# Optimization experiments

Measured on AMD Instinct MI355X. Metric: run time of the kernel, lower is better.

## Reference

```python
import jax, jax.numpy as jnp
import numpy as np

B, C1, C2, H, W = 4, 96, 96, 40, 40
DE, DI, R, N, K, E, TOPK = 192, 192, 6, 16, 4, 4, 2
EPS_BN = 1e-5
EPS_LN = 1e-5


def conv1x1(x, w):
    # x: (B,C,H,W), w: (O,C)
    return jnp.einsum('bchw,oc->bohw', x, w)


def dwconv3(x, w, b):
    # depthwise 3x3, w: (C,1,3,3)
    C = x.shape[1]
    y = jax.lax.conv_general_dilated(x, w, (1, 1), 'SAME',
                                     dimension_numbers=('NCHW', 'OIHW', 'NCHW'),
                                     feature_group_count=C)
    return y + b[None, :, None, None]


def bn_eval(x, g, b):
    # BatchNorm2d in eval mode with running_mean=0, running_var=1
    s = g / jnp.sqrt(1.0 + EPS_BN)
    return x * s[None, :, None, None] + b[None, :, None, None]


def layernorm(x, g, b):
    m = x.mean(-1, keepdims=True)
    xc = x - m
    v = (xc * xc).mean(-1, keepdims=True)
    return xc / jnp.sqrt(v + EPS_LN) * g + b


def gelu(x):
    return jax.nn.gelu(x, approximate=False)


def selective_scan(xs, dts, As, Bs, Cs):
    # xs, dts: (B,K,D,L); As: (K,D,N); Bs, Cs: (B,K,N,L)
    Bb, Kk, Dd, L = xs.shape
    Nn = As.shape[-1]
    xs_l = jnp.moveaxis(xs, -1, 0)   # (L,B,K,D)
    dts_l = jnp.moveaxis(dts, -1, 0)
    Bs_l = jnp.moveaxis(Bs, -1, 0)   # (L,B,K,N)
    Cs_l = jnp.moveaxis(Cs, -1, 0)
    h0 = jnp.zeros((Bb, Kk, Dd, Nn), xs.dtype)

    def step(h, inp):
        x_t, dt_t, B_t, C_t = inp
        dA = jnp.exp(dt_t[..., None] * As)                  # (B,K,D,N)
        h = h * dA + (dt_t * x_t)[..., None] * B_t[:, :, None, :]
        y = jnp.einsum('bkdn,bkn->bkd', h, C_t)
        return h, y

    _, ys = jax.lax.scan(step, h0, (xs_l, dts_l, Bs_l, Cs_l))
    return jnp.moveaxis(ys, 0, -1)   # (B,K,D,L)


def ss2d(x, in_proj_w, conv_w, conv_b, x_proj_w, dt_w, dt_b, A_logs, Ds,
         onorm_g, onorm_b, out_proj_w):
    # x: (B, C2, H, W)
    xz = conv1x1(x, in_proj_w)                      # (B, 2*DE, H, W)
    xx, z = jnp.split(xz, 2, axis=1)
    z1 = gelu(z)
    xx = gelu(dwconv3(xx, conv_w, conv_b))          # (B, DE, H, W)

    Bb, Dd, Hh, Ww = xx.shape
    L = Hh * Ww
    x_hw = xx.reshape(Bb, Dd, L)
    x_wh = xx.transpose(0, 1, 3, 2).reshape(Bb, Dd, L)
    xs = jnp.stack([x_hw, x_wh, x_hw[..., ::-1], x_wh[..., ::-1]], axis=1)  # (B,K,D,L)

    x_dbl = jnp.einsum('bkdl,kcd->bkcl', xs, x_proj_w)
    dts_r = x_dbl[:, :, :R]
    Bs = x_dbl[:, :, R:R + N]
    Cs = x_dbl[:, :, R + N:]
    dts = jnp.einsum('bkrl,kdr->bkdl', dts_r, dt_w)
    dts = jax.nn.softplus(dts + dt_b[None, :, :, None])
    As = -jnp.exp(A_logs.reshape(K, Dd, N))

    ys = selective_scan(xs, dts, As, Bs, Cs)
    ys = ys + Ds.reshape(K, Dd)[None, :, :, None] * xs

    # CrossMerge
    y = ys[:, 0] + ys[:, 2, :, ::-1]
    y_wh = ys[:, 1] + ys[:, 3, :, ::-1]
    y = y + y_wh.reshape(Bb, Dd, Ww, Hh).transpose(0, 1, 3, 2).reshape(Bb, Dd, L)

    y = layernorm(y.transpose(0, 2, 1), onorm_g, onorm_b)   # (B,L,D)
    y = y.reshape(Bb, Hh, Ww, Dd).transpose(0, 3, 1, 2)     # (B,D,H,W)
    y = y * z1
    return conv1x1(y, out_proj_w)


def moe(x, router_w, router_b, dw_w, dw_b, pw_w, pw_b):
    Bb = x.shape[0]
    g = x.mean(axis=(2, 3))                                 # (B,C)
    logits = g @ router_w.T + router_b
    prob = jax.nn.softmax(logits / 2.0, axis=-1)
    tp, ti = jax.lax.top_k(prob, TOPK)
    tp = tp / tp.sum(-1, keepdims=True)
    wmat = jnp.zeros((Bb, E), x.dtype).at[jnp.arange(Bb)[:, None], ti].add(tp)
    out = jnp.zeros_like(x)
    for e in range(E):
        h = gelu(dwconv3(x, dw_w[e], dw_b[e]))
        h = conv1x1(h, pw_w[e]) + pw_b[e][None, :, None, None]
        out = out + wmat[:, e][:, None, None, None] * h
    return out


def _forward(x, proj_w, bn0_g, bn0_b, ls_fc1_w, ls_fc1_b, ls_bn_g, ls_bn_b,
             ls_fc2_w, ls_fc2_b, ls_fc3_w, ls_fc3_b, n1_g, n1_b,
             in_proj_w, conv_w, conv_b, x_proj_w, dt_w, dt_b, A_logs, Ds,
             onorm_g, onorm_b, out_proj_w, n2_g, n2_b,
             router_w, router_b, moe_dw_w, moe_dw_b, moe_pw_w, moe_pw_b):
    x = jax.nn.silu(bn_eval(conv1x1(x, proj_w), bn0_g, bn0_b))
    res1 = x
    # LSBlock
    h = dwconv3(x, ls_fc1_w, ls_fc1_b)
    h = bn_eval(h, ls_bn_g, ls_bn_b)
    h = conv1x1(h, ls_fc2_w) + ls_fc2_b[None, :, None, None]
    h = gelu(h)
    h = conv1x1(h, ls_fc3_w) + ls_fc3_b[None, :, None, None]
    x1 = x + h
    x1 = ss2d(bn_eval(x1, n1_g, n1_b), in_proj_w, conv_w, conv_b, x_proj_w,
              dt_w, dt_b, A_logs, Ds, onorm_g, onorm_b, out_proj_w)
    x = res1 + x1
    x2 = moe(bn_eval(x, n2_g, n2_b), router_w, router_b,
             moe_dw_w, moe_dw_b, moe_pw_w, moe_pw_b)
    return x + x2


def setup_inputs() -> dict:
    key = jax.random.key(0)
    ks = jax.random.split(key, 16)
    rn = lambda k, shape, s: jax.random.normal(k, shape, jnp.float32) * s
    ones = lambda *s: jnp.ones(s, jnp.float32)
    zeros = lambda *s: jnp.zeros(s, jnp.float32)
    return {
        'x': jax.random.normal(ks[0], (B, C1, H, W), jnp.float32),
        'proj_w': rn(ks[1], (C2, C1), 0.1),
        'bn0_g': ones(C2), 'bn0_b': zeros(C2),
        'ls_fc1_w': rn(ks[2], (C2, 1, 3, 3), 0.2), 'ls_fc1_b': zeros(C2),
        'ls_bn_g': ones(C2), 'ls_bn_b': zeros(C2),
        'ls_fc2_w': rn(ks[3], (C2, C2), 0.1), 'ls_fc2_b': zeros(C2),
        'ls_fc3_w': rn(ks[4], (C2, C2), 0.1), 'ls_fc3_b': zeros(C2),
        'n1_g': ones(C2), 'n1_b': zeros(C2),
        'in_proj_w': rn(ks[5], (2 * DE, C2), 0.1),
        'conv_w': rn(ks[6], (DE, 1, 3, 3), 0.2), 'conv_b': zeros(DE),
        'x_proj_w': rn(ks[7], (K, R + 2 * N, DI), 0.1),
        'dt_w': rn(ks[8], (K, DI, R), 0.3),
        'dt_b': rn(ks[9], (K, DI), 0.5),
        'A_logs': rn(ks[10], (K * DI, N), 0.5),
        'Ds': ones(K * DI),
        'onorm_g': ones(DI), 'onorm_b': zeros(DI),
        'out_proj_w': rn(ks[11], (C2, DE), 0.1),
        'n2_g': ones(C2), 'n2_b': zeros(C2),
        'router_w': rn(ks[12], (E, C2), 0.1), 'router_b': zeros(E),
        'moe_dw_w': rn(ks[13], (E, C2, 1, 3, 3), 0.2), 'moe_dw_b': zeros(E, C2),
        'moe_pw_w': rn(ks[14], (E, C2, C2), 0.1), 'moe_pw_b': zeros(E, C2),
    }


def reference(x, proj_w, bn0_g, bn0_b, ls_fc1_w, ls_fc1_b, ls_bn_g, ls_bn_b,
              ls_fc2_w, ls_fc2_b, ls_fc3_w, ls_fc3_b, n1_g, n1_b,
              in_proj_w, conv_w, conv_b, x_proj_w, dt_w, dt_b, A_logs, Ds,
              onorm_g, onorm_b, out_proj_w, n2_g, n2_b,
              router_w, router_b, moe_dw_w, moe_dw_b, moe_pw_w, moe_pw_b):
    return _forward(x, proj_w, bn0_g, bn0_b, ls_fc1_w, ls_fc1_b, ls_bn_g, ls_bn_b,
                    ls_fc2_w, ls_fc2_b, ls_fc3_w, ls_fc3_b, n1_g, n1_b,
                    in_proj_w, conv_w, conv_b, x_proj_w, dt_w, dt_b, A_logs, Ds,
                    onorm_g, onorm_b, out_proj_w, n2_g, n2_b,
                    router_w, router_b, moe_dw_w, moe_dw_b, moe_pw_w, moe_pw_b)
```

## Files before the change

### kernel.cpp

```cpp
#include <hip/hip_runtime.h>
#include <hip/hip_bf16.h>
#include <math.h>

#define BB 4
#define CC 96
#define LL 1600
#define DD 192
#define KK 4
#define RR 6
#define NN 16
#define EE 4
#define NCH 40
#define CLEN 40

typedef __hip_bfloat16 bf16;

__device__ __forceinline__ float geluf(float x){ return 0.5f*x*(1.0f+erff(x*0.70710678118654752440f)); }
__device__ __forceinline__ float softplusf(float x){ return (x>20.0f)? x : __logf(1.0f+__expf(x)); }
#define BNS rsqrtf(1.0f + 1e-5f)
#define LOG2E 1.44269504088896340736f

__device__ __forceinline__ int xpos(int k, int l){
  if (k==0) return l;
  if (k==2) return LL-1-l;
  int t = (k==1)? l : (LL-1-l);
  return (t%40)*40 + t/40;
}

struct P33 { const void* p[33]; };
#define NTOT 790660
__device__ const int g_cum[34] = {
  0, 614400, 623616, 623712, 623808, 624672, 624768, 624864, 624960,
  634176, 634272, 643488, 643584, 643680, 643776, 680640, 682368, 682560,
  711744, 716352, 717120, 729408, 730176, 730368, 730560, 748992, 749088,
  749184, 749568, 749572, 753028, 753412, 790276, 790660
};

__global__ void k_convert(P33 ps, float* cv){
  bool f32 = (((const unsigned*)ps.p[21])[0] == 0x3F800000u);
  int idx = blockIdx.x*256 + threadIdx.x;
  if (idx >= NTOT) return;
  int lo=0, hi=33;
  while (lo+1<hi){ int mid=(lo+hi)>>1; if (idx >= g_cum[mid]) lo=mid; else hi=mid; }
  int local = idx - g_cum[lo];
  float v = f32 ? ((const float*)ps.p[lo])[local]
                : __bfloat162float(((const bf16*)ps.p[lo])[local]);
  cv[idx] = v;
}

__global__ void k_proj(const float* x, const float* w, const float* g, const float* b_, float* out){
  __shared__ float lx[96*64];
  int bid = blockIdx.x;
  int ot = bid%3, lt = (bid/3)%25, b = bid/75;
  int l0 = lt*64, ob = ot*32;
  const float* inb = x + b*CC*LL;
  for (int i=threadIdx.x; i<96*64; i+=256) lx[i] = inb[(i>>6)*LL + l0 + (i&63)];
  __syncthreads();
  int oq = threadIdx.x>>5, lq = threadIdx.x&31;
  float acc[4][2] = {};
  #pragma unroll 4
  for (int c=0;c<96;c++){
    float x0 = lx[c*64+lq], x1 = lx[c*64+lq+32];
    #pragma unroll
    for (int jo=0;jo<4;jo++){
      float wv = w[(ob+oq+8*jo)*CC + c];
      acc[jo][0] += wv*x0; acc[jo][1] += wv*x1;
    }
  }
  #pragma unroll
  for (int jo=0;jo<4;jo++){
    int o = ob+oq+8*jo;
    float sc = g[o]*BNS, bb = b_[o];
    #pragma unroll
    for (int jl=0;jl<2;jl++){
      float v = acc[jo][jl]*sc + bb;
      out[(b*CC+o)*LL + l0+lq+32*jl] = v/(1.0f+__expf(-v));
    }
  }
}

__global__ void k_fc_gelu(const float* in, const float* w, const float* bias, float* out){
  __shared__ float lx[96*64];
  int bid = blockIdx.x;
  int ot = bid%3, lt = (bid/3)%25, b = bid/75;
  int l0 = lt*64, ob = ot*32;
  const float* inb = in + b*CC*LL;
  for (int i=threadIdx.x; i<96*64; i+=256) lx[i] = inb[(i>>6)*LL + l0 + (i&63)];
  __syncthreads();
  int oq = threadIdx.x>>5, lq = threadIdx.x&31;
  float acc[4][2] = {};
  #pragma unroll 4
  for (int c=0;c<96;c++){
    float x0 = lx[c*64+lq], x1 = lx[c*64+lq+32];
    #pragma unroll
    for (int jo=0;jo<4;jo++){
      float wv = w[(ob+oq+8*jo)*CC + c];
      acc[jo][0] += wv*x0; acc[jo][1] += wv*x1;
    }
  }
  #pragma unroll
  for (int jo=0;jo<4;jo++){
    int o = ob+oq+8*jo;
    float bb = bias[o];
    out[(b*CC+o)*LL + l0+lq]    = geluf(acc[jo][0]+bb);
    out[(b*CC+o)*LL + l0+lq+32] = geluf(acc[jo][1]+bb);
  }
}

__global__ void k_fc_res_bn(const float* in, const float* w, const float* bias, const float* res,
                            const float* g, const float* b_, float* out){
  __shared__ float lx[96*64];
  int bid = blockIdx.x;
  int ot = bid%3, lt = (bid/3)%25, b = bid/75;
  int l0 = lt*64, ob = ot*32;
  const float* inb = in + b*CC*LL;
  for (int i=threadIdx.x; i<96*64; i+=256) lx[i] = inb[(i>>6)*LL + l0 + (i&63)];
  __syncthreads();
  int oq = threadIdx.x>>5, lq = threadIdx.x&31;
  float acc[4][2] = {};
  #pragma unroll 4
  for (int c=0;c<96;c++){
    float x0 = lx[c*64+lq], x1 = lx[c*64+lq+32];
    #pragma unroll
    for (int jo=0;jo<4;jo++){
      float wv = w[(ob+oq+8*jo)*CC + c];
      acc[jo][0] += wv*x0; acc[jo][1] += wv*x1;
    }
  }
  #pragma unroll
  for (int jo=0;jo<4;jo++){
    int o = ob+oq+8*jo;
    float bb = bias[o], sc = g[o]*BNS, b2 = b_[o];
    #pragma unroll
    for (int jl=0;jl<2;jl++){
      int pos = (b*CC+o)*LL + l0+lq+32*jl;
      float v = acc[jo][jl] + bb + res[pos];
      out[pos] = v*sc + b2;
    }
  }
}

__global__ void k_inproj(const float* in, const float* w, float* xxp, float* z1){
  __shared__ float lx[96*64];
  int bid = blockIdx.x;
  int ot = bid%12, lt = (bid/12)%25, b = bid/300;
  int l0 = lt*64, ob = ot*32;
  const float* inb = in + b*CC*LL;
  for (int i=threadIdx.x; i<96*64; i+=256) lx[i] = inb[(i>>6)*LL + l0 + (i&63)];
  __syncthreads();
  int oq = threadIdx.x>>5, lq = threadIdx.x&31;
  float acc[4][2] = {};
  #pragma unroll 4
  for (int c=0;c<96;c++){
    float x0 = lx[c*64+lq], x1 = lx[c*64+lq+32];
    #pragma unroll
    for (int jo=0;jo<4;jo++){
      float wv = w[(ob+oq+8*jo)*CC + c];
      acc[jo][0] += wv*x0; acc[jo][1] += wv*x1;
    }
  }
  if (ot < 6){
    #pragma unroll
    for (int jo=0;jo<4;jo++){
      int oc = ob+oq+8*jo;
      xxp[(b*DD+oc)*LL + l0+lq]    = acc[jo][0];
      xxp[(b*DD+oc)*LL + l0+lq+32] = acc[jo][1];
    }
  } else {
    __syncthreads();
    #pragma unroll
    for (int jo=0;jo<4;jo++){
      int oo = oq+8*jo;
      lx[lq*33 + oo]      = geluf(acc[jo][0]);
      lx[(lq+32)*33 + oo] = geluf(acc[jo][1]);
    }
    __syncthreads();
    int zb = ob - 192;
    for (int i=threadIdx.x; i<64*32; i+=256){
      int u = i>>5, oo = i&31;
      z1[(b*LL + l0+u)*DD + zb + oo] = lx[u*33 + oo];
    }
  }
}

__global__ void k_ssconv(const float* in, const float* w, const float* bias, float* out){
  int idx = blockIdx.x*256 + threadIdx.x;
  if (idx >= BB*DD*LL) return;
  int l = idx%LL, d = (idx/LL)%DD, b = idx/(LL*DD);
  int y = l/40, x0 = l%40;
  const float* ip = in + (b*DD+d)*LL;
  float acc = 0.f;
  #pragma unroll
  for (int ky=0;ky<3;ky++){
    int yy = y+ky-1; if (yy<0||yy>=40) continue;
    #pragma unroll
    for (int kx=0;kx<3;kx++){
      int xx = x0+kx-1; if (xx<0||xx>=40) continue;
      acc += w[d*9+ky*3+kx] * ip[yy*40+xx];
    }
  }
  out[idx] = geluf(acc + bias[d]);
}

__global__ void k_dwbn(const float* in, const float* w, const float* bias, const float* g, const float* b_, float* out){
  int idx = blockIdx.x*256 + threadIdx.x;
  if (idx >= BB*CC*LL) return;
  int l = idx%LL, c = (idx/LL)%CC, b = idx/(LL*CC);
  int y = l/40, x0 = l%40;
  const float* ip = in + (b*CC+c)*LL;
  float acc = 0.f;
  #pragma unroll
  for (int ky=0;ky<3;ky++){
    int yy = y+ky-1; if (yy<0||yy>=40) continue;
    #pragma unroll
    for (int kx=0;kx<3;kx++){
      int xx = x0+kx-1; if (xx<0||xx>=40) continue;
      acc += w[c*9+ky*3+kx] * ip[yy*40+xx];
    }
  }
  acc += bias[c];
  out[idx] = acc*(g[c]*BNS) + b_[c];
}

__global__ void k_xs(const float* xx, float* xs){
  __shared__ float t[32][33];
  int bid = blockIdx.x;
  int lt = bid % 50, dt = (bid/50)%6, b = bid/300;
  int l0 = lt*32, d0 = dt*32;
  int tx = threadIdx.x & 31, ty = threadIdx.x >> 5;
  #pragma unroll
  for (int j=0;j<4;j++){
    int dd = ty + 8*j;
    t[dd][tx] = xx[(b*DD + d0+dd)*LL + l0 + tx];
  }
  __syncthreads();
  #pragma unroll
  for (int j=0;j<4;j++){
    int ll = ty + 8*j;
    int l = l0 + ll;
    float v = t[tx][ll];
    int lw = (l%40)*40 + l/40;
    xs[((b*2+0)*LL + l )*DD + d0 + tx] = v;
    xs[((b*2+1)*LL + lw)*DD + d0 + tx] = v;
  }
}

__global__ void k_xw(const float* xx, float* xw1){
  __shared__ float sm[40*41];
  int bd = blockIdx.x;
  const float* ip = xx + bd*LL;
  float* op = xw1 + bd*LL;
  for (int i=threadIdx.x; i<LL; i+=256) sm[(i/40)*41 + (i%40)] = ip[i];
  __syncthreads();
  for (int i=threadIdx.x; i<LL; i+=256) op[i] = sm[(i%40)*41 + (i/40)];
}

__global__ void k_xdbl(const float* xx, const float* xw1, const float* w, float* xd){
  __shared__ float lt_[64*41];
  int bid = blockIdx.x;
  int tt = bid % 25, bk = bid / 25;
  int k = bk & 3, b = bk >> 2;
  int t0 = tt*64;
  int cg = threadIdx.x >> 6, tl = threadIdx.x & 63;
  int t = t0 + tl;
  int row = (k<2)? t : (LL-1-t);
  const float* base = ((k&1)? xw1 : xx) + b*DD*LL + row;
  const float* wp[10];
  #pragma unroll
  for (int j=0;j<10;j++){
    int c = cg + 4*j; if (c>37) c = 37;
    wp[j] = w + (k*38+c)*DD;
  }
  float acc[10] = {};
  for (int d=0; d<DD; d++){
    float xv = base[d*LL];
    #pragma unroll
    for (int j=0;j<10;j++) acc[j] += wp[j][d]*xv;
  }
  #pragma unroll
  for (int j=0;j<10;j++){
    int c = cg + 4*j;
    if (c < 38) lt_[tl*41 + c] = acc[j];
  }
  __syncthreads();
  float* ob = xd + (bk*LL + t0)*38;
  for (int i=threadIdx.x; i<64*38; i+=256) ob[i] = lt_[(i/38)*41 + (i%38)];
}

__global__ void k_scan1(const float* xs, const float* xd, const float* dtw, const float* dtb,
                        const float* Alog, float* Pb, float* Sb){
  int idx = blockIdx.x*256 + threadIdx.x;
  int lane = idx & 63;
  int d16 = lane & 15, g = lane >> 4;
  int wv_ = (idx>>6) % 12;
  int rest = (idx>>6) / 12;
  int c = rest % NCH, bk = rest / NCH;
  int d = wv_*16 + d16;
  int k = bk & 3, b = bk >> 2;
  int kd = k*DD + d;
  float w6[RR];
  #pragma unroll
  for (int r=0;r<RR;r++) w6[r] = dtw[kd*RR+r];
  float bias = dtb[kd];
  float A2[4], P[4]={1.f,1.f,1.f,1.f}, S[4]={0.f,0.f,0.f,0.f};
  #pragma unroll
  for (int n=0;n<4;n++) A2[n] = -expf(Alog[kd*NN + g*4 + n])*LOG2E;
  const float* xsb = xs + ((b*2)+(k&1))*LL*DD;
  const float* xr = xd + (bk*LL + c*CLEN)*38;
  bool rev = (k>=2);
  int t0 = c*CLEN;
  for (int j=0;j<CLEN;j++){
    int t = t0+j;
    int row = rev? (LL-1-t) : t;
    float dtr = bias;
    #pragma unroll
    for (int r=0;r<RR;r++) dtr += w6[r]*xr[r];
    float dt = softplusf(dtr);
    float xv = xsb[row*DD + d];
    float u = dt*xv;
    #pragma unroll
    for (int n=0;n<4;n++){
      float dA = exp2f(dt*A2[n]);
      P[n] *= dA;
      S[n] = S[n]*dA + u*xr[RR + g*4 + n];
    }
    xr += 38;
  }
  int off = ((bk*DD + d)*NCH + c)*NN + g*4;
  *(float4*)(Pb+off) = make_float4(P[0],P[1],P[2],P[3]);
  *(float4*)(Sb+off) = make_float4(S[0],S[1],S[2],S[3]);
}

__global__ void k_scanmid(float* Pb, const float* Sb){
  int idx = blockIdx.x*256 + threadIdx.x;
  if (idx >= BB*KK*DD*NN) return;
  int n = idx%NN, bkd = idx/NN;
  float h = 0.f;
  for (int c=0;c<NCH;c++){
    int o = (bkd*NCH + c)*NN + n;
    float p = Pb[o], s = Sb[o];
    Pb[o] = h;
    h = p*h + s;
  }
}

__global__ void k_scan2(const float* xs, const float* xd, const float* dtw, const float* dtb,
                        const float* Alog, const float* Hin, const float* Ds, float* Y){
  int idx = blockIdx.x*256 + threadIdx.x;
  int lane = idx & 63;
  int d16 = lane & 15, g = lane >> 4;
  int wv_ = (idx>>6) % 12;
  int rest = (idx>>6) / 12;
  int c = rest % NCH, bk = rest / NCH;
  int d = wv_*16 + d16;
  int k = bk & 3, b = bk >> 2;
  int kd = k*DD + d;
  float w6[RR];
  #pragma unroll
  for (int r=0;r<RR;r++) w6[r] = dtw[kd*RR+r];
  float bias = dtb[kd];
  int off = ((bk*DD + d)*NCH + c)*NN + g*4;
  float4 h4 = *(const float4*)(Hin+off);
  float h[4] = {h4.x, h4.y, h4.z, h4.w};
  float A2[4];
  #pragma unroll
  for (int n=0;n<4;n++) A2[n] = -expf(Alog[kd*NN + g*4 + n])*LOG2E;
  float Dv = Ds[kd];
  const float* xsb = xs + ((b*2)+(k&1))*LL*DD;
  const float* xr = xd + (bk*LL + c*CLEN)*38;
  float* yb = Y + b*LL*DD;
  bool rev = (k>=2);
  int t0 = c*CLEN;
  for (int j=0;j<CLEN;j++){
    int t = t0+j;
    int row = rev? (LL-1-t) : t;
    float dtr = bias;
    #pragma unroll
    for (int r=0;r<RR;r++) dtr += w6[r]*xr[r];
    float dt = softplusf(dtr);
    float xv = xsb[row*DD + d];
    float u = dt*xv;
    float y = 0.f;
    #pragma unroll
    for (int n=0;n<4;n++){
      float dA = exp2f(dt*A2[n]);
      h[n] = h[n]*dA + u*xr[RR + g*4 + n];
      y += h[n]*xr[RR + NN + g*4 + n];
    }
    y += __shfl_xor(y, 16, 64);
    y += __shfl_xor(y, 32, 64);
    if (g==0){
      int p = xpos(k, t);
      atomicAdd(&yb[p*DD + d], y + Dv*xv);
    }
    xr += 38;
  }
}

__global__ void k_ln(const float* Y, const float* og, const float* ob, const float* z1, float* yz){
  int r = blockIdx.x*4 + (threadIdx.x >> 6);
  int lane = threadIdx.x & 63;
  const float* yp = Y + r*DD;
  float v0 = yp[lane], v1 = yp[lane+64], v2 = yp[lane+128];
  float s = v0+v1+v2;
  #pragma unroll
  for (int off=32; off>0; off>>=1) s += __shfl_xor(s, off, 64);
  float m = s*(1.0f/DD);
  float t0=v0-m, t1=v1-m, t2=v2-m;
  float vv = t0*t0+t1*t1+t2*t2;
  #pragma unroll
  for (int off=32; off>0; off>>=1) vv += __shfl_xor(vv, off, 64);
  float rs = rsqrtf(vv*(1.0f/DD) + 1e-5f);
  #pragma unroll
  for (int i=0;i<3;i++){
    int d = lane + 64*i;
    float t = (i==0?t0:(i==1?t1:t2));
    yz[r*DD + d] = (t*rs*og[d] + ob[d]) * z1[r*DD + d];
  }
}

__global__ void k_outproj(const float* yz, const float* w, const float* res, const float* g, const float* b_,
                          float* x2, float* xb){
  __shared__ float lx[64*193];
  int bid = blockIdx.x;
  int ot = bid%3, lt = (bid/3)%25, b = bid/75;
  int l0 = lt*64, ob = ot*32;
  const float* src = yz + (b*LL + l0)*DD;
  for (int i=threadIdx.x; i<64*192; i+=256) lx[(i/192)*193 + (i%192)] = src[i];
  __syncthreads();
  int oq = threadIdx.x>>5, lq = threadIdx.x&31;
  float acc[4][2] = {};
  #pragma unroll 4
  for (int c=0;c<192;c++){
    float x0 = lx[lq*193 + c], x1 = lx[(lq+32)*193 + c];
    #pragma unroll
    for (int jo=0;jo<4;jo++){
      float wv = w[(ob+oq+8*jo)*DD + c];
      acc[jo][0] += wv*x0; acc[jo][1] += wv*x1;
    }
  }
  #pragma unroll
  for (int jo=0;jo<4;jo++){
    int o = ob+oq+8*jo;
    float sc = g[o]*BNS, b2 = b_[o];
    #pragma unroll
    for (int jl=0;jl<2;jl++){
      int pos = (b*CC+o)*LL + l0+lq+32*jl;
      float v = res[pos] + acc[jo][jl];
      x2[pos] = v;
      xb[pos] = v*sc + b2;
    }
  }
}

__global__ void k_gmean(const float* xb, float* gv){
  __shared__ float sm[4];
  int bc = blockIdx.x;
  int tid = threadIdx.x;
  const float* p = xb + bc*LL;
  float s = 0.f;
  for (int l=tid; l<LL; l+=256) s += p[l];
  #pragma unroll
  for (int off=32; off>0; off>>=1) s += __shfl_xor(s, off, 64);
  if ((tid&63)==0) sm[tid>>6] = s;
  __syncthreads();
  if (tid==0) gv[bc] = (sm[0]+sm[1]+sm[2]+sm[3])*(1.0f/LL);
}

__global__ void k_router(const float* gv, const float* rw, const float* rb, float* wm){
  int b = threadIdx.x;
  if (b >= BB) return;
  float lg[EE];
  for (int e=0;e<EE;e++){
    float a = rb[e];
    for (int c=0;c<CC;c++) a += gv[b*CC+c]*rw[e*CC+c];
    lg[e] = a*0.5f;
  }
  float mx = lg[0];
  for (int e=1;e<EE;e++) mx = fmaxf(mx, lg[e]);
  float p[EE], s = 0.f;
  for (int e=0;e<EE;e++){ p[e] = __expf(lg[e]-mx); s += p[e]; }
  for (int e=0;e<EE;e++) p[e] /= s;
  int i1 = 0;
  for (int e=1;e<EE;e++) if (p[e] > p[i1]) i1 = e;
  int i2 = -1;
  for (int e=0;e<EE;e++){ if (e==i1) continue; if (i2<0 || p[e]>p[i2]) i2 = e; }
  float tot = p[i1]+p[i2];
  for (int e=0;e<EE;e++) wm[b*EE+e] = 0.f;
  wm[b*EE+i1] = p[i1]/tot;
  wm[b*EE+i2] = p[i2]/tot;
}

__global__ void k_moedw(const float* xb, const float* dw, const float* db, const float* wm, float* he){
  int idx = blockIdx.x*256 + threadIdx.x;
  if (idx >= EE*BB*CC*LL) return;
  int l = idx%LL, c = (idx/LL)%CC, b = (idx/(LL*CC))%BB, e = idx/(LL*CC*BB);
  if (wm[b*EE+e] == 0.f) return;
  int y = l/40, x0 = l%40;
  const float* ip = xb + (b*CC+c)*LL;
  float acc = 0.f;
  #pragma unroll
  for (int ky=0;ky<3;ky++){
    int yy = y+ky-1; if (yy<0||yy>=40) continue;
    #pragma unroll
    for (int kx=0;kx<3;kx++){
      int xx = x0+kx-1; if (xx<0||xx>=40) continue;
      acc += dw[(e*CC+c)*9+ky*3+kx] * ip[yy*40+xx];
    }
  }
  he[((e*BB+b)*CC+c)*LL+l] = geluf(acc + db[e*CC+c]);
}

__global__ void k_final(const float* he, const float* pw, const float* pb, const float* wm,
                        const float* x2, void* out, const void* dsraw){
  __shared__ float lx[96*64];
  bool f32 = (((const unsigned*)dsraw)[0] == 0x3F800000u);
  int bid = blockIdx.x;
  int ot = bid%3, lt = (bid/3)%25, b = bid/75;
  int l0 = lt*64, ob = ot*32;
  int oq = threadIdx.x>>5, lq = threadIdx.x&31;
  float acc[4][2] = {};
  float bias[4] = {0.f,0.f,0.f,0.f};
  for (int e=0;e<EE;e++){
    float wv = wm[b*EE+e];
    if (wv == 0.f) continue;
    __syncthreads();
    const float* hb = he + (e*BB+b)*CC*LL;
    for (int i=threadIdx.x; i<96*64; i+=256) lx[i] = hb[(i>>6)*LL + l0 + (i&63)];
    __syncthreads();
    float ae[4][2] = {};
    #pragma unroll 4
    for (int c=0;c<96;c++){
      float x0 = lx[c*64+lq], x1 = lx[c*64+lq+32];
      #pragma unroll
      for (int jo=0;jo<4;jo++){
        float wvw = pw[(e*CC+ob+oq+8*jo)*CC + c];
        ae[jo][0] += wvw*x0; ae[jo][1] += wvw*x1;
      }
    }
    #pragma unroll
    for (int jo=0;jo<4;jo++){
      acc[jo][0] += wv*ae[jo][0];
      acc[jo][1] += wv*ae[jo][1];
      bias[jo] += wv*pb[e*CC+ob+oq+8*jo];
    }
  }
  #pragma unroll
  for (int jo=0;jo<4;jo++){
    int o = ob+oq+8*jo;
    #pragma unroll
    for (int jl=0;jl<2;jl++){
      int pos = (b*CC+o)*LL + l0+lq+32*jl;
      float v = x2[pos] + acc[jo][jl] + bias[jo];
      if (f32) ((float*)out)[pos] = v;
      else     ((bf16*)out)[pos] = __float2bfloat16(v);
    }
  }
}

extern "C" void kernel_launch(void* const* d_in, const int* in_sizes, int n_in,
                              void* d_out, int out_size, void* d_ws, size_t ws_size,
                              hipStream_t stream) {
  static const int cum[34] = {
    0, 614400, 623616, 623712, 623808, 624672, 624768, 624864, 624960,
    634176, 634272, 643488, 643584, 643680, 643776, 680640, 682368, 682560,
    711744, 716352, 717120, 729408, 730176, 730368, 730560, 748992, 749088,
    749184, 749568, 749572, 753028, 753412, 790276, 790660
  };
  float* ws = (float*)d_ws;
  const float* cv[33];
  P33 ps;
  for (int i=0;i<33;i++){ ps.p[i] = d_in[i]; cv[i] = ws + cum[i]; }

  const float* c_x    = cv[0];
  const float* c_pw   = cv[1];
  const float* c_bn0g = cv[2];
  const float* c_bn0b = cv[3];
  const float* c_f1w  = cv[4];
  const float* c_f1b  = cv[5];
  const float* c_lbg  = cv[6];
  const float* c_lbb  = cv[7];
  const float* c_f2w  = cv[8];
  const float* c_f2b  = cv[9];
  const float* c_f3w  = cv[10];
  const float* c_f3b  = cv[11];
  const float* c_n1g  = cv[12];
  const float* c_n1b  = cv[13];
  const float* c_ipw  = cv[14];
  const float* c_cw   = cv[15];
  const float* c_cb   = cv[16];
  const float* c_xpw  = cv[17];
  const float* c_dtw  = cv[18];
  const float* c_dtb  = cv[19];
  const float* c_al   = cv[20];
  const float* c_ds   = cv[21];
  const float* c_ong  = cv[22];
  const float* c_onb  = cv[23];
  const float* c_opw  = cv[24];
  const float* c_n2g  = cv[25];
  const float* c_n2b  = cv[26];
  const float* c_rw   = cv[27];
  const float* c_rb   = cv[28];
  const float* c_mdw  = cv[29];
  const float* c_mdb  = cv[30];
  const float* c_mpw  = cv[31];
  const float* c_mpb  = cv[32];

  float* R   = ws +   790784;
  float* T1  = ws +  1405184;
  float* X1  = T1;
  float* X2  = T1;
  float* T2  = ws +  2019584;
  float* XB  = T2;
  float* XW1 = T1;
  float* XXP = ws +  2633984;
  float* Y   = XXP;
  float* Z1  = ws +  3862784;
  float* XX  = ws +  5091584;
  float* YZ  = XX;
  float* XS  = ws +  6320384;
  float* HE  = XS;
  float* XD  = ws +  8777984;
  float* GV  = XD;
  float* WM  = XD + 384;
  float* PB  = ws +  9750784;
  float* SB  = ws + 11716864;

  const int T = 256;
  k_convert  <<<(NTOT+T-1)/T, T, 0, stream>>>(ps, ws);
  k_proj     <<<300, T, 0, stream>>>(c_x, c_pw, c_bn0g, c_bn0b, R);
  k_dwbn     <<<(BB*CC*LL+T-1)/T, T, 0, stream>>>(R, c_f1w, c_f1b, c_lbg, c_lbb, T1);
  k_fc_gelu  <<<300, T, 0, stream>>>(T1, c_f2w, c_f2b, T2);
  k_fc_res_bn<<<300, T, 0, stream>>>(T2, c_f3w, c_f3b, R, c_n1g, c_n1b, X1);
  k_inproj   <<<1200, T, 0, stream>>>(X1, c_ipw, XXP, Z1);
  k_ssconv   <<<(BB*DD*LL+T-1)/T, T, 0, stream>>>(XXP, c_cw, c_cb, XX);
  k_xs       <<<1200, T, 0, stream>>>(XX, XS);
  k_xw       <<<BB*DD, T, 0, stream>>>(XX, XW1);
  hipMemsetAsync(Y, 0, (size_t)BB*DD*LL*sizeof(float), stream);
  k_xdbl     <<<BB*KK*25, T, 0, stream>>>(XX, XW1, c_xpw, XD);
  k_scan1    <<<(BB*KK*NCH*768)/T, T, 0, stream>>>(XS, XD, c_dtw, c_dtb, c_al, PB, SB);
  k_scanmid  <<<(BB*KK*DD*NN+T-1)/T, T, 0, stream>>>(PB, SB);
  k_scan2    <<<(BB*KK*NCH*768)/T, T, 0, stream>>>(XS, XD, c_dtw, c_dtb, c_al, PB, c_ds, Y);
  k_ln       <<<1600, T, 0, stream>>>(Y, c_ong, c_onb, Z1, YZ);
  k_outproj  <<<300, T, 0, stream>>>(YZ, c_opw, R, c_n2g, c_n2b, X2, XB);
  k_gmean    <<<BB*CC, T, 0, stream>>>(XB, GV);
  k_router   <<<1, 64, 0, stream>>>(GV, c_rw, c_rb, WM);
  k_moedw    <<<(EE*BB*CC*LL+T-1)/T, T, 0, stream>>>(XB, c_mdw, c_mdb, WM, HE);
  k_final    <<<300, T, 0, stream>>>(HE, c_mpw, c_mpb, WM, X2, d_out, d_in[21]);
}
```

Measured before the change: 442.2 us.

## Pad x_dbl rows to 40, precompute dt in shared memory, fuse MoE depthwise experts

The x_dbl buffer is re-laid out with a stride of 40 floats, with B/C first and the dt rank columns moved to offset 32, so the scan kernels can use aligned float4 loads for B and C. Both scan passes now compute softplus(dt) once per (d, timestep) into shared memory per block, so it is no longer recomputed by all four n-group lanes. The x_dbl projection uses smaller tiles (32 timesteps), doubling the block count. The MoE depthwise kernel loads the 3x3 neighbourhood once and loops over the selected experts, instead of launching one thread per expert.

```diff
diff --git a/kernel.cpp b/kernel.cpp
--- a/kernel.cpp
+++ b/kernel.cpp
@@ -256,75 +256,91 @@
 }
 
 __global__ void k_xdbl(const float* xx, const float* xw1, const float* w, float* xd){
-  __shared__ float lt_[64*41];
-  int bid = blockIdx.x;
-  int tt = bid % 25, bk = bid / 25;
+  __shared__ float lt_[32*41];
+  int bid = blockIdx.x;
+  int tt = bid % 50, bk = bid / 50;
   int k = bk & 3, b = bk >> 2;
-  int t0 = tt*64;
-  int cg = threadIdx.x >> 6, tl = threadIdx.x & 63;
+  int t0 = tt*32;
+  int cg = threadIdx.x >> 5, tl = threadIdx.x & 31;
   int t = t0 + tl;
   int row = (k<2)? t : (LL-1-t);
   const float* base = ((k&1)? xw1 : xx) + b*DD*LL + row;
-  const float* wp[10];
-  #pragma unroll
-  for (int j=0;j<10;j++){
-    int c = cg + 4*j; if (c>37) c = 37;
+  const float* wp[5];
+  #pragma unroll
+  for (int j=0;j<5;j++){
+    int c = cg + 8*j; if (c>37) c = 37;
     wp[j] = w + (k*38+c)*DD;
   }
-  float acc[10] = {};
+  float acc[5] = {};
   for (int d=0; d<DD; d++){
     float xv = base[d*LL];
     #pragma unroll
-    for (int j=0;j<10;j++) acc[j] += wp[j][d]*xv;
-  }
-  #pragma unroll
-  for (int j=0;j<10;j++){
-    int c = cg + 4*j;
+    for (int j=0;j<5;j++) acc[j] += wp[j][d]*xv;
+  }
+  #pragma unroll
+  for (int j=0;j<5;j++){
+    int c = cg + 8*j;
     if (c < 38) lt_[tl*41 + c] = acc[j];
   }
   __syncthreads();
-  float* ob = xd + (bk*LL + t0)*38;
-  for (int i=threadIdx.x; i<64*38; i+=256) ob[i] = lt_[(i/38)*41 + (i%38)];
+  float* ob = xd + (bk*LL + t0)*40;
+  for (int i=threadIdx.x; i<32*40; i+=256){
+    int tr = i/40, col = i%40;
+    float v;
+    if (col < 32)      v = lt_[tr*41 + col + 6];
+    else if (col < 38) v = lt_[tr*41 + col - 32];
+    else               v = 0.f;
+    ob[i] = v;
+  }
 }
 
 __global__ void k_scan1(const float* xs, const float* xd, const float* dtw, const float* dtb,
                         const float* Alog, float* Pb, float* Sb){
-  int idx = blockIdx.x*256 + threadIdx.x;
-  int lane = idx & 63;
+  __shared__ float ldt[64*41];
+  int bid = blockIdx.x;
+  int dt3 = bid % 3;
+  int c   = (bid/3) % NCH;
+  int bk  = bid/(3*NCH);
+  int k = bk & 3, b = bk >> 2;
+  int d0 = dt3*64;
+  const float* xrow0 = xd + (bk*LL + c*CLEN)*40;
+  for (int i=threadIdx.x; i<64*CLEN; i+=256){
+    int dd = i/CLEN, j = i%CLEN;
+    int kd = k*DD + d0 + dd;
+    const float* r = xrow0 + j*40 + 32;
+    float dtr = dtb[kd];
+    #pragma unroll
+    for (int q=0;q<RR;q++) dtr += dtw[kd*RR+q]*r[q];
+    ldt[dd*41 + j] = softplusf(dtr);
+  }
+  __syncthreads();
+  int lane = threadIdx.x & 63;
   int d16 = lane & 15, g = lane >> 4;
-  int wv_ = (idx>>6) % 12;
-  int rest = (idx>>6) / 12;
-  int c = rest % NCH, bk = rest / NCH;
-  int d = wv_*16 + d16;
-  int k = bk & 3, b = bk >> 2;
+  int dd = (threadIdx.x>>6)*16 + d16;
+  int d = d0 + dd;
   int kd = k*DD + d;
-  float w6[RR];
-  #pragma unroll
-  for (int r=0;r<RR;r++) w6[r] = dtw[kd*RR+r];
-  float bias = dtb[kd];
   float A2[4], P[4]={1.f,1.f,1.f,1.f}, S[4]={0.f,0.f,0.f,0.f};
   #pragma unroll
   for (int n=0;n<4;n++) A2[n] = -expf(Alog[kd*NN + g*4 + n])*LOG2E;
   const float* xsb = xs + ((b*2)+(k&1))*LL*DD;
-  const float* xr = xd + (bk*LL + c*CLEN)*38;
   bool rev = (k>=2);
   int t0 = c*CLEN;
+  const float* xr = xrow0;
   for (int j=0;j<CLEN;j++){
     int t = t0+j;
     int row = rev? (LL-1-t) : t;
-    float dtr = bias;
-    #pragma unroll
-    for (int r=0;r<RR;r++) dtr += w6[r]*xr[r];
-    float dt = softplusf(dtr);
+    float dt = ldt[dd*41 + j];
+    float4 B4 = *(const float4*)(xr + g*4);
     float xv = xsb[row*DD + d];
     float u = dt*xv;
+    float Ba[4] = {B4.x,B4.y,B4.z,B4.w};
     #pragma unroll
     for (int n=0;n<4;n++){
       float dA = exp2f(dt*A2[n]);
       P[n] *= dA;
-      S[n] = S[n]*dA + u*xr[RR + g*4 + n];
-    }
-    xr += 38;
+      S[n] = S[n]*dA + u*Ba[n];
+    }
+    xr += 40;
   }
   int off = ((bk*DD + d)*NCH + c)*NN + g*4;
   *(float4*)(Pb+off) = make_float4(P[0],P[1],P[2],P[3]);
@@ -346,19 +362,29 @@
 
 __global__ void k_scan2(const float* xs, const float* xd, const float* dtw, const float* dtb,
                         const float* Alog, const float* Hin, const float* Ds, float* Y){
-  int idx = blockIdx.x*256 + threadIdx.x;
-  int lane = idx & 63;
+  __shared__ float ldt[64*41];
+  int bid = blockIdx.x;
+  int dt3 = bid % 3;
+  int c   = (bid/3) % NCH;
+  int bk  = bid/(3*NCH);
+  int k = bk & 3, b = bk >> 2;
+  int d0 = dt3*64;
+  const float* xrow0 = xd + (bk*LL + c*CLEN)*40;
+  for (int i=threadIdx.x; i<64*CLEN; i+=256){
+    int dd = i/CLEN, j = i%CLEN;
+    int kd = k*DD + d0 + dd;
+    const float* r = xrow0 + j*40 + 32;
+    float dtr = dtb[kd];
+    #pragma unroll
+    for (int q=0;q<RR;q++) dtr += dtw[kd*RR+q]*r[q];
+    ldt[dd*41 + j] = softplusf(dtr);
+  }
+  __syncthreads();
+  int lane = threadIdx.x & 63;
   int d16 = lane & 15, g = lane >> 4;
-  int wv_ = (idx>>6) % 12;
-  int rest = (idx>>6) / 12;
-  int c = rest % NCH, bk = rest / NCH;
-  int d = wv_*16 + d16;
-  int k = bk & 3, b = bk >> 2;
+  int dd = (threadIdx.x>>6)*16 + d16;
+  int d = d0 + dd;
   int kd = k*DD + d;
-  float w6[RR];
-  #pragma unroll
-  for (int r=0;r<RR;r++) w6[r] = dtw[kd*RR+r];
-  float bias = dtb[kd];
   int off = ((bk*DD + d)*NCH + c)*NN + g*4;
   float4 h4 = *(const float4*)(Hin+off);
   float h[4] = {h4.x, h4.y, h4.z, h4.w};
@@ -367,25 +393,26 @@
   for (int n=0;n<4;n++) A2[n] = -expf(Alog[kd*NN + g*4 + n])*LOG2E;
   float Dv = Ds[kd];
   const float* xsb = xs + ((b*2)+(k&1))*LL*DD;
-  const float* xr = xd + (bk*LL + c*CLEN)*38;
   float* yb = Y + b*LL*DD;
   bool rev = (k>=2);
   int t0 = c*CLEN;
+  const float* xr = xrow0;
   for (int j=0;j<CLEN;j++){
     int t = t0+j;
     int row = rev? (LL-1-t) : t;
-    float dtr = bias;
-    #pragma unroll
-    for (int r=0;r<RR;r++) dtr += w6[r]*xr[r];
-    float dt = softplusf(dtr);
+    float dt = ldt[dd*41 + j];
+    float4 B4 = *(const float4*)(xr + g*4);
+    float4 C4 = *(const float4*)(xr + 16 + g*4);
     float xv = xsb[row*DD + d];
     float u = dt*xv;
+    float Ba[4] = {B4.x,B4.y,B4.z,B4.w};
+    float Ca[4] = {C4.x,C4.y,C4.z,C4.w};
     float y = 0.f;
     #pragma unroll
     for (int n=0;n<4;n++){
       float dA = exp2f(dt*A2[n]);
-      h[n] = h[n]*dA + u*xr[RR + g*4 + n];
-      y += h[n]*xr[RR + NN + g*4 + n];
+      h[n] = h[n]*dA + u*Ba[n];
+      y += h[n]*Ca[n];
     }
     y += __shfl_xor(y, 16, 64);
     y += __shfl_xor(y, 32, 64);
@@ -393,7 +420,7 @@
       int p = xpos(k, t);
       atomicAdd(&yb[p*DD + d], y + Dv*xv);
     }
-    xr += 38;
+    xr += 40;
   }
 }
 
@@ -493,22 +520,29 @@
 
 __global__ void k_moedw(const float* xb, const float* dw, const float* db, const float* wm, float* he){
   int idx = blockIdx.x*256 + threadIdx.x;
-  if (idx >= EE*BB*CC*LL) return;
-  int l = idx%LL, c = (idx/LL)%CC, b = (idx/(LL*CC))%BB, e = idx/(LL*CC*BB);
-  if (wm[b*EE+e] == 0.f) return;
+  if (idx >= BB*CC*LL) return;
+  int l = idx%LL, c = (idx/LL)%CC, b = idx/(LL*CC);
   int y = l/40, x0 = l%40;
   const float* ip = xb + (b*CC+c)*LL;
-  float acc = 0.f;
+  float v[9];
   #pragma unroll
   for (int ky=0;ky<3;ky++){
-    int yy = y+ky-1; if (yy<0||yy>=40) continue;
     #pragma unroll
     for (int kx=0;kx<3;kx++){
-      int xx = x0+kx-1; if (xx<0||xx>=40) continue;
-      acc += dw[(e*CC+c)*9+ky*3+kx] * ip[yy*40+xx];
-    }
-  }
-  he[((e*BB+b)*CC+c)*LL+l] = geluf(acc + db[e*CC+c]);
+      int yy=y+ky-1, xx=x0+kx-1;
+      v[ky*3+kx] = (yy<0||yy>=40||xx<0||xx>=40)? 0.f : ip[yy*40+xx];
+    }
+  }
+  #pragma unroll
+  for (int e=0;e<EE;e++){
+    float wv = wm[b*EE+e];
+    if (wv == 0.f) continue;
+    const float* wp = dw + (e*CC+c)*9;
+    float acc = db[e*CC+c];
+    #pragma unroll
+    for (int q=0;q<9;q++) acc += wp[q]*v[q];
+    he[((e*BB+b)*CC+c)*LL+l] = geluf(acc);
+  }
 }
 
 __global__ void k_final(const float* he, const float* pw, const float* pb, const float* wm,
@@ -623,8 +657,8 @@
   float* XD  = ws +  8777984;
   float* GV  = XD;
   float* WM  = XD + 384;
-  float* PB  = ws +  9750784;
-  float* SB  = ws + 11716864;
+  float* PB  = ws +  9801984;
+  float* SB  = ws + 11768064;
 
   const int T = 256;
   k_convert  <<<(NTOT+T-1)/T, T, 0, stream>>>(ps, ws);
@@ -637,14 +671,14 @@
   k_xs       <<<1200, T, 0, stream>>>(XX, XS);
   k_xw       <<<BB*DD, T, 0, stream>>>(XX, XW1);
   hipMemsetAsync(Y, 0, (size_t)BB*DD*LL*sizeof(float), stream);
-  k_xdbl     <<<BB*KK*25, T, 0, stream>>>(XX, XW1, c_xpw, XD);
-  k_scan1    <<<(BB*KK*NCH*768)/T, T, 0, stream>>>(XS, XD, c_dtw, c_dtb, c_al, PB, SB);
+  k_xdbl     <<<BB*KK*50, T, 0, stream>>>(XX, XW1, c_xpw, XD);
+  k_scan1    <<<BB*KK*NCH*3, T, 0, stream>>>(XS, XD, c_dtw, c_dtb, c_al, PB, SB);
   k_scanmid  <<<(BB*KK*DD*NN+T-1)/T, T, 0, stream>>>(PB, SB);
-  k_scan2    <<<(BB*KK*NCH*768)/T, T, 0, stream>>>(XS, XD, c_dtw, c_dtb, c_al, PB, c_ds, Y);
+  k_scan2    <<<BB*KK*NCH*3, T, 0, stream>>>(XS, XD, c_dtw, c_dtb, c_al, PB, c_ds, Y);
   k_ln       <<<1600, T, 0, stream>>>(Y, c_ong, c_onb, Z1, YZ);
   k_outproj  <<<300, T, 0, stream>>>(YZ, c_opw, R, c_n2g, c_n2b, X2, XB);
   k_gmean    <<<BB*CC, T, 0, stream>>>(XB, GV);
   k_router   <<<1, 64, 0, stream>>>(GV, c_rw, c_rb, WM);
-  k_moedw    <<<(EE*BB*CC*LL+T-1)/T, T, 0, stream>>>(XB, c_mdw, c_mdb, WM, HE);
+  k_moedw    <<<(BB*CC*LL+T-1)/T, T, 0, stream>>>(XB, c_mdw, c_mdb, WM, HE);
   k_final    <<<300, T, 0, stream>>>(HE, c_mpw, c_mpb, WM, X2, d_out, d_in[21]);
 }
```

New measurement: 411.4 us. 1.07x faster.
